# Optimization experiments

Measured on AMD Instinct MI355X. Metric: run time of the kernel, lower is better.

## Reference

```python
import jax, jax.numpy as jnp
import numpy as np

N_SRC = 100000
N_DST = 50000
N_EDGES = 1600000
D_IN = 128
D_OUT = 64


def setup_inputs() -> dict:
    key = jax.random.key(0)
    ks = jax.random.split(key, 6)
    x = jax.random.normal(ks[0], (N_SRC, D_IN), dtype=jnp.float32)
    W_l = jax.random.normal(ks[1], (D_IN, D_OUT), dtype=jnp.float32) * (1.0 / np.sqrt(D_IN))
    b_l = jax.random.normal(ks[2], (D_OUT,), dtype=jnp.float32) * 0.01
    W_r = jax.random.normal(ks[3], (D_IN, D_OUT), dtype=jnp.float32) * (1.0 / np.sqrt(D_IN))
    src = jax.random.randint(ks[4], (N_EDGES,), 0, N_SRC, dtype=jnp.int64)
    dst = jax.random.randint(ks[5], (N_EDGES,), 0, N_DST, dtype=jnp.int64)
    edge_index = jnp.stack([src, dst], axis=0)
    return {"x": x, "W_l": W_l, "b_l": b_l, "W_r": W_r,
            "edge_index": edge_index, "n_dst": N_DST}


def reference(x, W_l, b_l, W_r, edge_index, n_dst):
    src, dst = edge_index[0], edge_index[1]
    # gather source features along edges: [E, D_in]
    msgs = x[src]
    # mean aggregation at destination nodes
    agg = jax.ops.segment_sum(msgs, dst, num_segments=n_dst)          # [n_dst, D_in]
    cnt = jax.ops.segment_sum(jnp.ones_like(dst, dtype=x.dtype), dst,
                              num_segments=n_dst)                     # [n_dst]
    mean = agg / jnp.maximum(cnt, 1.0)[:, None]
    x_target = x[:n_dst]
    # SAGEConv: lin_l(mean_agg) + lin_r(x_target)
    out = mean @ W_l + b_l + x_target @ W_r                           # [n_dst, D_out]
    return jax.nn.log_softmax(out, axis=-1)
```

## Files before the change

### kernel.cpp

```cpp
#include <hip/hip_runtime.h>
#include <math.h>

#define DIN  128
#define DOUT 64
#define PROWS 64
#define XPITCH 132
#define BSH  7
#define BMSK 127
#define BCAP 4672

__device__ inline unsigned short f2bf(float f) {
    unsigned u = __float_as_uint(f);
    u += 0x7fffu + ((u >> 16) & 1u);
    return (unsigned short)(u >> 16);
}
__device__ inline float bflo(unsigned u) { return __uint_as_float(u << 16); }
__device__ inline float bfhi(unsigned u) { return __uint_as_float(u & 0xffff0000u); }

__global__ void __launch_bounds__(256) build_k(
    const int* __restrict__ ei, unsigned* __restrict__ gTail,
    int* __restrict__ bucketBuf,
    const float* __restrict__ x, const float* __restrict__ Wl,
    const float* __restrict__ bl, const float* __restrict__ Wr,
    unsigned short* __restrict__ y, float* __restrict__ zout,
    int E, int nFill, int P, int nyb, int n_src, int n_dst, int nB)
{
    __shared__ float s_x[PROWS * XPITCH];
    const int b = blockIdx.x;
    const int fq = b / P;
    const bool isFill = ((b % P) == 0) && (fq < nFill);

    if (isFill) {
        int* s_i  = (int*)s_x;
        int* lcnt = s_i;
        int* lpos = s_i + 512;
        int* s_gb = s_i + 1024;
        const int t = threadIdx.x;
        const int myb = (fq * 256 + t) * 8;
        const bool full = (myb + 8 <= E);
        const bool any  = (myb < E);
        int4 sa, sb4, da, db;
        if (full) {
            sa  = *(const int4*)(ei + myb);
            sb4 = *(const int4*)(ei + myb + 4);
            da  = *(const int4*)(ei + E + myb);
            db  = *(const int4*)(ei + E + myb + 4);
        }
        lcnt[t] = 0; lcnt[t + 256] = 0;
        lpos[t] = 0; lpos[t + 256] = 0;
        __syncthreads();
        if (full) {
            atomicAdd(&lcnt[da.x >> BSH], 1); atomicAdd(&lcnt[da.y >> BSH], 1);
            atomicAdd(&lcnt[da.z >> BSH], 1); atomicAdd(&lcnt[da.w >> BSH], 1);
            atomicAdd(&lcnt[db.x >> BSH], 1); atomicAdd(&lcnt[db.y >> BSH], 1);
            atomicAdd(&lcnt[db.z >> BSH], 1); atomicAdd(&lcnt[db.w >> BSH], 1);
        } else if (any) {
            for (int i = myb; i < E && i < myb + 8; ++i)
                atomicAdd(&lcnt[ei[E + i] >> BSH], 1);
        }
        __syncthreads();
        for (int bk = t; bk < nB; bk += 256)
            s_gb[bk] = (int)atomicAdd(&gTail[bk], (unsigned)lcnt[bk]);
        __syncthreads();
#define PLACE(S, D) { int bk = (D) >> BSH; int p = atomicAdd(&lpos[bk], 1);          \
                      unsigned pos = (unsigned)(s_gb[bk] + p);                        \
                      if (pos < BCAP) bucketBuf[(size_t)bk * BCAP + pos] =            \
                          ((S) << BSH) | ((D) & BMSK); }
        if (full) {
            PLACE(sa.x,  da.x) PLACE(sa.y,  da.y) PLACE(sa.z,  da.z) PLACE(sa.w,  da.w)
            PLACE(sb4.x, db.x) PLACE(sb4.y, db.y) PLACE(sb4.z, db.z) PLACE(sb4.w, db.w)
        } else if (any) {
            for (int i = myb; i < E && i < myb + 8; ++i) {
                int s = ei[i], d = ei[E + i];
                PLACE(s, d)
            }
        }
#undef PLACE
        return;
    }

    const int fillsBefore = (fq + 1 < nFill) ? (fq + 1) : nFill;
    const int pb = b - fillsBefore;
    const int t  = threadIdx.x;
    const bool isY = (pb < nyb);
    const int rowBase = (isY ? pb : pb - nyb) * PROWS;
    const int nRows = isY ? n_src : n_dst;
    const float* __restrict__ W = isY ? Wl : Wr;

    {
        const float* xsrc = x + (size_t)rowBase * DIN;
        #pragma unroll
        for (int j = 0; j < 8; ++j) {
            int fi  = t + 256 * j;
            int row = fi >> 5, c4 = fi & 31;
            if (rowBase + row < nRows) {
                float4 v = *(const float4*)(xsrc + (size_t)fi * 4);
                *(float4*)(&s_x[row * XPITCH + c4 * 4]) = v;
            }
        }
    }
    __syncthreads();

    const int cg = t & 15;
    const int rg = t >> 4;
    const int r0 = rg * 4;
    const float* wp = W + cg * 4;

    float4 acc0 = {0.f,0.f,0.f,0.f};
    float4 acc1 = {0.f,0.f,0.f,0.f};
    float4 acc2 = {0.f,0.f,0.f,0.f};
    float4 acc3 = {0.f,0.f,0.f,0.f};

#define ROWFMA(acc, xv)                                                                     \
    acc.x = fmaf(xv.w, w3.x, fmaf(xv.z, w2.x, fmaf(xv.y, w1.x, fmaf(xv.x, w0.x, acc.x)))); \
    acc.y = fmaf(xv.w, w3.y, fmaf(xv.z, w2.y, fmaf(xv.y, w1.y, fmaf(xv.x, w0.y, acc.y)))); \
    acc.z = fmaf(xv.w, w3.z, fmaf(xv.z, w2.z, fmaf(xv.y, w1.z, fmaf(xv.x, w0.z, acc.z)))); \
    acc.w = fmaf(xv.w, w3.w, fmaf(xv.z, w2.w, fmaf(xv.y, w1.w, fmaf(xv.x, w0.w, acc.w))));

    #pragma unroll 2
    for (int k = 0; k < DIN; k += 4) {
        float4 w0 = *(const float4*)(wp + (size_t)(k + 0) * DOUT);
        float4 w1 = *(const float4*)(wp + (size_t)(k + 1) * DOUT);
        float4 w2 = *(const float4*)(wp + (size_t)(k + 2) * DOUT);
        float4 w3 = *(const float4*)(wp + (size_t)(k + 3) * DOUT);
        float4 x0 = *(const float4*)(&s_x[(r0 + 0) * XPITCH + k]);
        float4 x1 = *(const float4*)(&s_x[(r0 + 1) * XPITCH + k]);
        float4 x2 = *(const float4*)(&s_x[(r0 + 2) * XPITCH + k]);
        float4 x3 = *(const float4*)(&s_x[(r0 + 3) * XPITCH + k]);
        ROWFMA(acc0, x0)
        ROWFMA(acc1, x1)
        ROWFMA(acc2, x2)
        ROWFMA(acc3, x3)
    }
#undef ROWFMA

    if (isY) {
        float4 av[4] = {acc0, acc1, acc2, acc3};
        #pragma unroll
        for (int r = 0; r < 4; ++r) {
            int row = rowBase + r0 + r;
            if (row < nRows) {
                uint2 pk;
                pk.x = (unsigned)f2bf(av[r].x) | ((unsigned)f2bf(av[r].y) << 16);
                pk.y = (unsigned)f2bf(av[r].z) | ((unsigned)f2bf(av[r].w) << 16);
                *(uint2*)(y + (size_t)row * DOUT + cg * 4) = pk;
            }
        }
    } else {
        const float4 bv = *(const float4*)(bl + cg * 4);
        float4 av[4] = {acc0, acc1, acc2, acc3};
        #pragma unroll
        for (int r = 0; r < 4; ++r) {
            int row = rowBase + r0 + r;
            if (row < nRows) {
                float4 o;
                o.x = av[r].x + bv.x; o.y = av[r].y + bv.y;
                o.z = av[r].z + bv.z; o.w = av[r].w + bv.w;
                *(float4*)(zout + (size_t)row * DOUT + cg * 4) = o;
            }
        }
    }
}

__global__ void __launch_bounds__(512) bucket_k(
    const unsigned* __restrict__ gTail, const int* __restrict__ bucketBuf,
    int* __restrict__ rs, int* __restrict__ csr, int n_dst, int nB)
{
    __shared__ int s_ent[BCAP];
    __shared__ int s_hist[128];
    __shared__ int s_ofs[128];
    __shared__ int s_part[32];
    __shared__ int s_tails[512];
    __shared__ int s_bstart;
    const int b = blockIdx.x, t = threadIdx.x;
    const int lane = t & 63, wave = t >> 6;

    s_tails[t] = (t < nB) ? (int)gTail[t] : 0;
    if (t < 128) s_hist[t] = 0;
    __syncthreads();
    if (t == 0) {
        int acc = 0;
        for (int j = 0; j < b; ++j) {
            int v = s_tails[j];
            acc += (v < BCAP) ? v : BCAP;
        }
        s_bstart = acc;
    }
    int m = s_tails[b]; if (m > BCAP) m = BCAP;
    __syncthreads();

    const int* bb = bucketBuf + (size_t)b * BCAP;
    const int4* bb4 = (const int4*)bb;
    int4* se4 = (int4*)s_ent;
    const int m4 = m >> 2;
    for (int i4 = t; i4 < m4; i4 += 512) {
        int4 e4 = bb4[i4];
        se4[i4] = e4;
        atomicAdd(&s_hist[e4.x & BMSK], 1);
        atomicAdd(&s_hist[e4.y & BMSK], 1);
        atomicAdd(&s_hist[e4.z & BMSK], 1);
        atomicAdd(&s_hist[e4.w & BMSK], 1);
    }
    for (int i = (m4 << 2) + t; i < m; i += 512) {
        int e = bb[i];
        s_ent[i] = e;
        atomicAdd(&s_hist[e & BMSK], 1);
    }
    __syncthreads();

    if (t < 32) {
        s_part[t] = s_hist[4*t] + s_hist[4*t+1] + s_hist[4*t+2] + s_hist[4*t+3];
    }
    __syncthreads();
    if (wave == 0) {
        int v = (lane < 32) ? s_part[lane] : 0;
        for (int o = 1; o < 32; o <<= 1) {
            int u = __shfl_up(v, o);
            if (lane >= o) v += u;
        }
        if (lane < 32) s_part[lane] = v;
    }
    __syncthreads();
    if (t < 32) {
        int base = (t == 0) ? 0 : s_part[t-1];
        int h0 = s_hist[4*t], h1 = s_hist[4*t+1], h2 = s_hist[4*t+2];
        s_ofs[4*t]   = base;
        s_ofs[4*t+1] = base + h0;
        s_ofs[4*t+2] = base + h0 + h1;
        s_ofs[4*t+3] = base + h0 + h1 + h2;
    }
    __syncthreads();

    const int dbase = b << BSH;
    int nloc = n_dst - dbase; if (nloc > 128) nloc = 128;
    const int bstart = s_bstart;
    if (t < nloc) rs[dbase + t] = bstart + s_ofs[t];
    if (t == 0)   rs[dbase + nloc] = bstart + m;
    __syncthreads();

    for (int i4 = t; i4 < m4; i4 += 512) {
        int4 e4 = se4[i4];
        int p0 = atomicAdd(&s_ofs[e4.x & BMSK], 1); csr[bstart + p0] = e4.x >> BSH;
        int p1 = atomicAdd(&s_ofs[e4.y & BMSK], 1); csr[bstart + p1] = e4.y >> BSH;
        int p2 = atomicAdd(&s_ofs[e4.z & BMSK], 1); csr[bstart + p2] = e4.z >> BSH;
        int p3 = atomicAdd(&s_ofs[e4.w & BMSK], 1); csr[bstart + p3] = e4.w >> BSH;
    }
    for (int i = (m4 << 2) + t; i < m; i += 512) {
        int e = s_ent[i];
        int p = atomicAdd(&s_ofs[e & BMSK], 1);
        csr[bstart + p] = e >> BSH;
    }
}

__global__ void __launch_bounds__(256) gather_k(
    const unsigned short* __restrict__ y,
    const int* __restrict__ rs, const int* __restrict__ csr,
    float* __restrict__ out, int n_dst)
{
    const int wave = threadIdx.x >> 6, lane = threadIdx.x & 63;
    const int row = blockIdx.x * 4 + wave;
    if (row >= n_dst) return;

    const int start = rs[row];
    const int deg = rs[row + 1] - start;
    const int g  = lane >> 3;
    const int c8 = lane & 7;
    const uint4* yw = (const uint4*)y;

    const float4 zv0 = *(const float4*)(out + (size_t)row * DOUT + c8 * 8);
    const float4 zv1 = *(const float4*)(out + (size_t)row * DOUT + c8 * 8 + 4);

    float4 a0l = {0,0,0,0}, a0h = {0,0,0,0};
    float4 a1l = {0,0,0,0}, a1h = {0,0,0,0};
    float4 a2l = {0,0,0,0}, a2h = {0,0,0,0};
    float4 a3l = {0,0,0,0}, a3h = {0,0,0,0};
    const int* srow = csr + start;

#define ACC8(al, ah, u)                                              \
    al.x += bflo(u.x); al.y += bfhi(u.x);                            \
    al.z += bflo(u.y); al.w += bfhi(u.y);                            \
    ah.x += bflo(u.z); ah.y += bfhi(u.z);                            \
    ah.z += bflo(u.w); ah.w += bfhi(u.w);

    for (int co = 0; co < deg; co += 64) {
        int rem = deg - co; if (rem > 64) rem = 64;
        int idx = (lane < rem) ? srow[co + lane] : 0;
        int i = 0;
        for (; i + 32 <= rem; i += 32) {
            int s0 = __shfl(idx, i + g);
            int s1 = __shfl(idx, i + 8 + g);
            int s2 = __shfl(idx, i + 16 + g);
            int s3 = __shfl(idx, i + 24 + g);
            uint4 u0 = yw[(size_t)s0 * 8 + c8];
            uint4 u1 = yw[(size_t)s1 * 8 + c8];
            uint4 u2 = yw[(size_t)s2 * 8 + c8];
            uint4 u3 = yw[(size_t)s3 * 8 + c8];
            ACC8(a0l, a0h, u0)
            ACC8(a1l, a1h, u1)
            ACC8(a2l, a2h, u2)
            ACC8(a3l, a3h, u3)
        }
        for (; i < rem; i += 8) {
            int e = i + g;
            int s0 = __shfl(idx, e);
            if (e < rem) {
                uint4 u = yw[(size_t)s0 * 8 + c8];
                ACC8(a0l, a0h, u)
            }
        }
    }
#undef ACC8

    float4 sl, sh;
    sl.x = (a0l.x + a1l.x) + (a2l.x + a3l.x);
    sl.y = (a0l.y + a1l.y) + (a2l.y + a3l.y);
    sl.z = (a0l.z + a1l.z) + (a2l.z + a3l.z);
    sl.w = (a0l.w + a1l.w) + (a2l.w + a3l.w);
    sh.x = (a0h.x + a1h.x) + (a2h.x + a3h.x);
    sh.y = (a0h.y + a1h.y) + (a2h.y + a3h.y);
    sh.z = (a0h.z + a1h.z) + (a2h.z + a3h.z);
    sh.w = (a0h.w + a1h.w) + (a2h.w + a3h.w);

    #pragma unroll
    for (int o = 32; o >= 8; o >>= 1) {
        sl.x += __shfl_xor(sl.x, o); sl.y += __shfl_xor(sl.y, o);
        sl.z += __shfl_xor(sl.z, o); sl.w += __shfl_xor(sl.w, o);
        sh.x += __shfl_xor(sh.x, o); sh.y += __shfl_xor(sh.y, o);
        sh.z += __shfl_xor(sh.z, o); sh.w += __shfl_xor(sh.w, o);
    }

    const float scale = 1.0f / (float)(deg > 0 ? deg : 1);
    float4 v0, v1;
    v0.x = sl.x * scale + zv0.x; v0.y = sl.y * scale + zv0.y;
    v0.z = sl.z * scale + zv0.z; v0.w = sl.w * scale + zv0.w;
    v1.x = sh.x * scale + zv1.x; v1.y = sh.y * scale + zv1.y;
    v1.z = sh.z * scale + zv1.z; v1.w = sh.w * scale + zv1.w;

    float m = fmaxf(fmaxf(fmaxf(v0.x, v0.y), fmaxf(v0.z, v0.w)),
                    fmaxf(fmaxf(v1.x, v1.y), fmaxf(v1.z, v1.w)));
    for (int o = 4; o >= 1; o >>= 1) m = fmaxf(m, __shfl_xor(m, o));
    float s = expf(v0.x - m) + expf(v0.y - m) + expf(v0.z - m) + expf(v0.w - m)
            + expf(v1.x - m) + expf(v1.y - m) + expf(v1.z - m) + expf(v1.w - m);
    for (int o = 4; o >= 1; o >>= 1) s += __shfl_xor(s, o);
    const float lse = m + logf(s);

    if (lane < 8) {
        float4 o0, o1;
        o0.x = v0.x - lse; o0.y = v0.y - lse; o0.z = v0.z - lse; o0.w = v0.w - lse;
        o1.x = v1.x - lse; o1.y = v1.y - lse; o1.z = v1.z - lse; o1.w = v1.w - lse;
        *(float4*)(out + (size_t)row * DOUT + c8 * 8)     = o0;
        *(float4*)(out + (size_t)row * DOUT + c8 * 8 + 4) = o1;
    }
}

extern "C" void kernel_launch(void* const* d_in, const int* in_sizes, int n_in,
                              void* d_out, int out_size, void* d_ws, size_t ws_size,
                              hipStream_t stream)
{
    const float* x  = (const float*)d_in[0];
    const float* Wl = (const float*)d_in[1];
    const float* bl = (const float*)d_in[2];
    const float* Wr = (const float*)d_in[3];
    const int*   ei = (const int*)d_in[4];

    const int E     = in_sizes[4] / 2;
    const int n_src = in_sizes[0] / DIN;
    const int n_dst = out_size / DOUT;
    const int nB    = (n_dst + (1 << BSH) - 1) >> BSH;

    unsigned* gTail = (unsigned*)d_ws;
    int* rs  = (int*)d_ws + 512;
    int* csr = rs + (n_dst + 256);
    int* bucketBuf = csr + E;
    unsigned short* yb = (unsigned short*)(bucketBuf + (size_t)nB * BCAP);

    hipMemsetAsync(gTail, 0, 512 * sizeof(unsigned), stream);

    int nFill = (E + 2047) / 2048;
    int nyb = (n_src + PROWS - 1) / PROWS;
    int nzb = (n_dst + PROWS - 1) / PROWS;
    int total = nFill + nyb + nzb;
    int P = (total + nFill - 1) / nFill;

    build_k<<<total, 256, 0, stream>>>(
        ei, gTail, bucketBuf, x, Wl, bl, Wr, yb, (float*)d_out,
        E, nFill, P, nyb, n_src, n_dst, nB);

    bucket_k<<<nB, 512, 0, stream>>>(gTail, bucketBuf, rs, csr, n_dst, nB);

    int gG = (n_dst + 3) / 4;
    gather_k<<<gG, 256, 0, stream>>>(yb, rs, csr, (float*)d_out, n_dst);
}
```

Measured before the change: 218.1 us.

## Fuse bucket sort and gather into one kernel using LDS-resident CSR

Halves the bucket width to 64 destinations and merges the bucket-sort and gather kernels. Each block now sorts its bucket into shared memory and directly aggregates those 64 rows with 8 waves, so the global CSR and row-start arrays are never written or re-read and one launch is removed. The cost is fewer, larger blocks (about 782 blocks of 512 threads) with more shared memory each, which could lower occupancy and the parallelism available for latency hiding in the gather.

```diff
diff --git a/kernel.cpp b/kernel.cpp
--- a/kernel.cpp
+++ b/kernel.cpp
@@ -5,9 +5,9 @@
 #define DOUT 64
 #define PROWS 64
 #define XPITCH 132
-#define BSH  7
-#define BMSK 127
-#define BCAP 4672
+#define BSH  6
+#define BMSK 63
+#define BCAP 2496
 
 __device__ inline unsigned short f2bf(float f) {
     unsigned u = __float_as_uint(f);
@@ -33,8 +33,8 @@
     if (isFill) {
         int* s_i  = (int*)s_x;
         int* lcnt = s_i;
-        int* lpos = s_i + 512;
-        int* s_gb = s_i + 1024;
+        int* lpos = s_i + 1024;
+        int* s_gb = s_i + 2048;
         const int t = threadIdx.x;
         const int myb = (fq * 256 + t) * 8;
         const bool full = (myb + 8 <= E);
@@ -46,8 +46,8 @@
             da  = *(const int4*)(ei + E + myb);
             db  = *(const int4*)(ei + E + myb + 4);
         }
-        lcnt[t] = 0; lcnt[t + 256] = 0;
-        lpos[t] = 0; lpos[t + 256] = 0;
+        lcnt[t] = 0; lcnt[t + 256] = 0; lcnt[t + 512] = 0; lcnt[t + 768] = 0;
+        lpos[t] = 0; lpos[t + 256] = 0; lpos[t + 512] = 0; lpos[t + 768] = 0;
         __syncthreads();
         if (full) {
             atomicAdd(&lcnt[da.x >> BSH], 1); atomicAdd(&lcnt[da.y >> BSH], 1);
@@ -162,31 +162,21 @@
     }
 }
 
-__global__ void __launch_bounds__(512) bucket_k(
+__global__ void __launch_bounds__(512) bg_k(
     const unsigned* __restrict__ gTail, const int* __restrict__ bucketBuf,
-    int* __restrict__ rs, int* __restrict__ csr, int n_dst, int nB)
+    const unsigned short* __restrict__ y,
+    float* __restrict__ out, int n_dst)
 {
     __shared__ int s_ent[BCAP];
-    __shared__ int s_hist[128];
-    __shared__ int s_ofs[128];
-    __shared__ int s_part[32];
-    __shared__ int s_tails[512];
-    __shared__ int s_bstart;
+    __shared__ int s_csr[BCAP];
+    __shared__ int s_hist[64];
+    __shared__ int s_ofs[64];
+    __shared__ int s_start[65];
     const int b = blockIdx.x, t = threadIdx.x;
     const int lane = t & 63, wave = t >> 6;
 
-    s_tails[t] = (t < nB) ? (int)gTail[t] : 0;
-    if (t < 128) s_hist[t] = 0;
-    __syncthreads();
-    if (t == 0) {
-        int acc = 0;
-        for (int j = 0; j < b; ++j) {
-            int v = s_tails[j];
-            acc += (v < BCAP) ? v : BCAP;
-        }
-        s_bstart = acc;
-    }
-    int m = s_tails[b]; if (m > BCAP) m = BCAP;
+    if (t < 64) s_hist[t] = 0;
+    int m = (int)gTail[b]; if (m > BCAP) m = BCAP;
     __syncthreads();
 
     const int* bb = bucketBuf + (size_t)b * BCAP;
@@ -208,73 +198,38 @@
     }
     __syncthreads();
 
-    if (t < 32) {
-        s_part[t] = s_hist[4*t] + s_hist[4*t+1] + s_hist[4*t+2] + s_hist[4*t+3];
-    }
-    __syncthreads();
     if (wave == 0) {
-        int v = (lane < 32) ? s_part[lane] : 0;
-        for (int o = 1; o < 32; o <<= 1) {
+        int h = s_hist[lane];
+        int v = h;
+        for (int o = 1; o < 64; o <<= 1) {
             int u = __shfl_up(v, o);
             if (lane >= o) v += u;
         }
-        if (lane < 32) s_part[lane] = v;
-    }
-    __syncthreads();
-    if (t < 32) {
-        int base = (t == 0) ? 0 : s_part[t-1];
-        int h0 = s_hist[4*t], h1 = s_hist[4*t+1], h2 = s_hist[4*t+2];
-        s_ofs[4*t]   = base;
-        s_ofs[4*t+1] = base + h0;
-        s_ofs[4*t+2] = base + h0 + h1;
-        s_ofs[4*t+3] = base + h0 + h1 + h2;
-    }
-    __syncthreads();
-
-    const int dbase = b << BSH;
-    int nloc = n_dst - dbase; if (nloc > 128) nloc = 128;
-    const int bstart = s_bstart;
-    if (t < nloc) rs[dbase + t] = bstart + s_ofs[t];
-    if (t == 0)   rs[dbase + nloc] = bstart + m;
+        s_start[lane + 1] = v;
+        if (lane == 0) s_start[0] = 0;
+        s_ofs[lane] = v - h;
+    }
     __syncthreads();
 
     for (int i4 = t; i4 < m4; i4 += 512) {
         int4 e4 = se4[i4];
-        int p0 = atomicAdd(&s_ofs[e4.x & BMSK], 1); csr[bstart + p0] = e4.x >> BSH;
-        int p1 = atomicAdd(&s_ofs[e4.y & BMSK], 1); csr[bstart + p1] = e4.y >> BSH;
-        int p2 = atomicAdd(&s_ofs[e4.z & BMSK], 1); csr[bstart + p2] = e4.z >> BSH;
-        int p3 = atomicAdd(&s_ofs[e4.w & BMSK], 1); csr[bstart + p3] = e4.w >> BSH;
+        int p0 = atomicAdd(&s_ofs[e4.x & BMSK], 1); s_csr[p0] = e4.x >> BSH;
+        int p1 = atomicAdd(&s_ofs[e4.y & BMSK], 1); s_csr[p1] = e4.y >> BSH;
+        int p2 = atomicAdd(&s_ofs[e4.z & BMSK], 1); s_csr[p2] = e4.z >> BSH;
+        int p3 = atomicAdd(&s_ofs[e4.w & BMSK], 1); s_csr[p3] = e4.w >> BSH;
     }
     for (int i = (m4 << 2) + t; i < m; i += 512) {
         int e = s_ent[i];
         int p = atomicAdd(&s_ofs[e & BMSK], 1);
-        csr[bstart + p] = e >> BSH;
-    }
-}
-
-__global__ void __launch_bounds__(256) gather_k(
-    const unsigned short* __restrict__ y,
-    const int* __restrict__ rs, const int* __restrict__ csr,
-    float* __restrict__ out, int n_dst)
-{
-    const int wave = threadIdx.x >> 6, lane = threadIdx.x & 63;
-    const int row = blockIdx.x * 4 + wave;
-    if (row >= n_dst) return;
-
-    const int start = rs[row];
-    const int deg = rs[row + 1] - start;
+        s_csr[p] = e >> BSH;
+    }
+    __syncthreads();
+
+    const int dbase = b << BSH;
+    int nloc = n_dst - dbase; if (nloc > 64) nloc = 64;
     const int g  = lane >> 3;
     const int c8 = lane & 7;
     const uint4* yw = (const uint4*)y;
-
-    const float4 zv0 = *(const float4*)(out + (size_t)row * DOUT + c8 * 8);
-    const float4 zv1 = *(const float4*)(out + (size_t)row * DOUT + c8 * 8 + 4);
-
-    float4 a0l = {0,0,0,0}, a0h = {0,0,0,0};
-    float4 a1l = {0,0,0,0}, a1h = {0,0,0,0};
-    float4 a2l = {0,0,0,0}, a2h = {0,0,0,0};
-    float4 a3l = {0,0,0,0}, a3h = {0,0,0,0};
-    const int* srow = csr + start;
 
 #define ACC8(al, ah, u)                                              \
     al.x += bflo(u.x); al.y += bfhi(u.x);                            \
@@ -282,75 +237,89 @@
     ah.x += bflo(u.z); ah.y += bfhi(u.z);                            \
     ah.z += bflo(u.w); ah.w += bfhi(u.w);
 
-    for (int co = 0; co < deg; co += 64) {
-        int rem = deg - co; if (rem > 64) rem = 64;
-        int idx = (lane < rem) ? srow[co + lane] : 0;
-        int i = 0;
-        for (; i + 32 <= rem; i += 32) {
-            int s0 = __shfl(idx, i + g);
-            int s1 = __shfl(idx, i + 8 + g);
-            int s2 = __shfl(idx, i + 16 + g);
-            int s3 = __shfl(idx, i + 24 + g);
-            uint4 u0 = yw[(size_t)s0 * 8 + c8];
-            uint4 u1 = yw[(size_t)s1 * 8 + c8];
-            uint4 u2 = yw[(size_t)s2 * 8 + c8];
-            uint4 u3 = yw[(size_t)s3 * 8 + c8];
-            ACC8(a0l, a0h, u0)
-            ACC8(a1l, a1h, u1)
-            ACC8(a2l, a2h, u2)
-            ACC8(a3l, a3h, u3)
-        }
-        for (; i < rem; i += 8) {
-            int e = i + g;
-            int s0 = __shfl(idx, e);
-            if (e < rem) {
-                uint4 u = yw[(size_t)s0 * 8 + c8];
-                ACC8(a0l, a0h, u)
-            }
+    for (int r = wave; r < nloc; r += 8) {
+        const int row = dbase + r;
+        const int start = s_start[r];
+        const int deg = s_start[r + 1] - start;
+
+        const float4 zv0 = *(const float4*)(out + (size_t)row * DOUT + c8 * 8);
+        const float4 zv1 = *(const float4*)(out + (size_t)row * DOUT + c8 * 8 + 4);
+
+        float4 a0l = {0,0,0,0}, a0h = {0,0,0,0};
+        float4 a1l = {0,0,0,0}, a1h = {0,0,0,0};
+        float4 a2l = {0,0,0,0}, a2h = {0,0,0,0};
+        float4 a3l = {0,0,0,0}, a3h = {0,0,0,0};
+
+        for (int co = 0; co < deg; co += 64) {
+            int rem = deg - co; if (rem > 64) rem = 64;
+            int idx = (lane < rem) ? s_csr[start + co + lane] : 0;
+            int i = 0;
+            for (; i + 32 <= rem; i += 32) {
+                int s0 = __shfl(idx, i + g);
+                int s1 = __shfl(idx, i + 8 + g);
+                int s2 = __shfl(idx, i + 16 + g);
+                int s3 = __shfl(idx, i + 24 + g);
+                uint4 u0 = yw[(size_t)s0 * 8 + c8];
+                uint4 u1 = yw[(size_t)s1 * 8 + c8];
+                uint4 u2 = yw[(size_t)s2 * 8 + c8];
+                uint4 u3 = yw[(size_t)s3 * 8 + c8];
+                ACC8(a0l, a0h, u0)
+                ACC8(a1l, a1h, u1)
+                ACC8(a2l, a2h, u2)
+                ACC8(a3l, a3h, u3)
+            }
+            for (; i < rem; i += 8) {
+                int e = i + g;
+                int s0 = __shfl(idx, e);
+                if (e < rem) {
+                    uint4 u = yw[(size_t)s0 * 8 + c8];
+                    ACC8(a0l, a0h, u)
+                }
+            }
+        }
+
+        float4 sl, sh;
+        sl.x = (a0l.x + a1l.x) + (a2l.x + a3l.x);
+        sl.y = (a0l.y + a1l.y) + (a2l.y + a3l.y);
+        sl.z = (a0l.z + a1l.z) + (a2l.z + a3l.z);
+        sl.w = (a0l.w + a1l.w) + (a2l.w + a3l.w);
+        sh.x = (a0h.x + a1h.x) + (a2h.x + a3h.x);
+        sh.y = (a0h.y + a1h.y) + (a2h.y + a3h.y);
+        sh.z = (a0h.z + a1h.z) + (a2h.z + a3h.z);
+        sh.w = (a0h.w + a1h.w) + (a2h.w + a3h.w);
+
+        #pragma unroll
+        for (int o = 32; o >= 8; o >>= 1) {
+            sl.x += __shfl_xor(sl.x, o); sl.y += __shfl_xor(sl.y, o);
+            sl.z += __shfl_xor(sl.z, o); sl.w += __shfl_xor(sl.w, o);
+            sh.x += __shfl_xor(sh.x, o); sh.y += __shfl_xor(sh.y, o);
+            sh.z += __shfl_xor(sh.z, o); sh.w += __shfl_xor(sh.w, o);
+        }
+
+        const float scale = 1.0f / (float)(deg > 0 ? deg : 1);
+        float4 v0, v1;
+        v0.x = sl.x * scale + zv0.x; v0.y = sl.y * scale + zv0.y;
+        v0.z = sl.z * scale + zv0.z; v0.w = sl.w * scale + zv0.w;
+        v1.x = sh.x * scale + zv1.x; v1.y = sh.y * scale + zv1.y;
+        v1.z = sh.z * scale + zv1.z; v1.w = sh.w * scale + zv1.w;
+
+        float mx = fmaxf(fmaxf(fmaxf(v0.x, v0.y), fmaxf(v0.z, v0.w)),
+                         fmaxf(fmaxf(v1.x, v1.y), fmaxf(v1.z, v1.w)));
+        for (int o = 4; o >= 1; o >>= 1) mx = fmaxf(mx, __shfl_xor(mx, o));
+        float s = expf(v0.x - mx) + expf(v0.y - mx) + expf(v0.z - mx) + expf(v0.w - mx)
+                + expf(v1.x - mx) + expf(v1.y - mx) + expf(v1.z - mx) + expf(v1.w - mx);
+        for (int o = 4; o >= 1; o >>= 1) s += __shfl_xor(s, o);
+        const float lse = mx + logf(s);
+
+        if (lane < 8) {
+            float4 o0, o1;
+            o0.x = v0.x - lse; o0.y = v0.y - lse; o0.z = v0.z - lse; o0.w = v0.w - lse;
+            o1.x = v1.x - lse; o1.y = v1.y - lse; o1.z = v1.z - lse; o1.w = v1.w - lse;
+            *(float4*)(out + (size_t)row * DOUT + c8 * 8)     = o0;
+            *(float4*)(out + (size_t)row * DOUT + c8 * 8 + 4) = o1;
         }
     }
 #undef ACC8
-
-    float4 sl, sh;
-    sl.x = (a0l.x + a1l.x) + (a2l.x + a3l.x);
-    sl.y = (a0l.y + a1l.y) + (a2l.y + a3l.y);
-    sl.z = (a0l.z + a1l.z) + (a2l.z + a3l.z);
-    sl.w = (a0l.w + a1l.w) + (a2l.w + a3l.w);
-    sh.x = (a0h.x + a1h.x) + (a2h.x + a3h.x);
-    sh.y = (a0h.y + a1h.y) + (a2h.y + a3h.y);
-    sh.z = (a0h.z + a1h.z) + (a2h.z + a3h.z);
-    sh.w = (a0h.w + a1h.w) + (a2h.w + a3h.w);
-
-    #pragma unroll
-    for (int o = 32; o >= 8; o >>= 1) {
-        sl.x += __shfl_xor(sl.x, o); sl.y += __shfl_xor(sl.y, o);
-        sl.z += __shfl_xor(sl.z, o); sl.w += __shfl_xor(sl.w, o);
-        sh.x += __shfl_xor(sh.x, o); sh.y += __shfl_xor(sh.y, o);
-        sh.z += __shfl_xor(sh.z, o); sh.w += __shfl_xor(sh.w, o);
-    }
-
-    const float scale = 1.0f / (float)(deg > 0 ? deg : 1);
-    float4 v0, v1;
-    v0.x = sl.x * scale + zv0.x; v0.y = sl.y * scale + zv0.y;
-    v0.z = sl.z * scale + zv0.z; v0.w = sl.w * scale + zv0.w;
-    v1.x = sh.x * scale + zv1.x; v1.y = sh.y * scale + zv1.y;
-    v1.z = sh.z * scale + zv1.z; v1.w = sh.w * scale + zv1.w;
-
-    float m = fmaxf(fmaxf(fmaxf(v0.x, v0.y), fmaxf(v0.z, v0.w)),
-                    fmaxf(fmaxf(v1.x, v1.y), fmaxf(v1.z, v1.w)));
-    for (int o = 4; o >= 1; o >>= 1) m = fmaxf(m, __shfl_xor(m, o));
-    float s = expf(v0.x - m) + expf(v0.y - m) + expf(v0.z - m) + expf(v0.w - m)
-            + expf(v1.x - m) + expf(v1.y - m) + expf(v1.z - m) + expf(v1.w - m);
-    for (int o = 4; o >= 1; o >>= 1) s += __shfl_xor(s, o);
-    const float lse = m + logf(s);
-
-    if (lane < 8) {
-        float4 o0, o1;
-        o0.x = v0.x - lse; o0.y = v0.y - lse; o0.z = v0.z - lse; o0.w = v0.w - lse;
-        o1.x = v1.x - lse; o1.y = v1.y - lse; o1.z = v1.z - lse; o1.w = v1.w - lse;
-        *(float4*)(out + (size_t)row * DOUT + c8 * 8)     = o0;
-        *(float4*)(out + (size_t)row * DOUT + c8 * 8 + 4) = o1;
-    }
 }
 
 extern "C" void kernel_launch(void* const* d_in, const int* in_sizes, int n_in,
@@ -369,12 +338,10 @@
     const int nB    = (n_dst + (1 << BSH) - 1) >> BSH;
 
     unsigned* gTail = (unsigned*)d_ws;
-    int* rs  = (int*)d_ws + 512;
-    int* csr = rs + (n_dst + 256);
-    int* bucketBuf = csr + E;
+    int* bucketBuf = (int*)d_ws + 1024;
     unsigned short* yb = (unsigned short*)(bucketBuf + (size_t)nB * BCAP);
 
-    hipMemsetAsync(gTail, 0, 512 * sizeof(unsigned), stream);
+    hipMemsetAsync(gTail, 0, 1024 * sizeof(unsigned), stream);
 
     int nFill = (E + 2047) / 2048;
     int nyb = (n_src + PROWS - 1) / PROWS;
@@ -386,8 +353,5 @@
         ei, gTail, bucketBuf, x, Wl, bl, Wr, yb, (float*)d_out,
         E, nFill, P, nyb, n_src, n_dst, nB);
 
-    bucket_k<<<nB, 512, 0, stream>>>(gTail, bucketBuf, rs, csr, n_dst, nB);
-
-    int gG = (n_dst + 3) / 4;
-    gather_k<<<gG, 256, 0, stream>>>(yb, rs, csr, (float*)d_out, n_dst);
+    bg_k<<<nB, 512, 0, stream>>>(gTail, bucketBuf, yb, (float*)d_out, n_dst);
 }
```

After: 209.4 us. 1.04x faster.
